# Kernel optimization log

Hardware: AMD Instinct MI355X
Metric: run time of the kernel (lower is better)

Reference implementation:

```python
import jax, jax.numpy as jnp
import numpy as np

N = 262144          # batch size
C = 100             # num_classes
R0, R1 = 0.95, 1.0  # recall_range
LAM = 0.5           # lambda_pauc
LS = 0.1            # label_smoothing
MAX_PAUC = R1 - R0


def setup_inputs() -> dict:
    key = jax.random.key(0)
    k1, k2 = jax.random.split(key)
    predictions = jax.random.normal(k1, (N, C), dtype=jnp.float32)
    targets = jax.random.randint(k2, (N,), 0, C)
    weight = jnp.ones((C,), dtype=jnp.float32)
    return {"predictions": predictions, "targets": targets, "weight": weight}


def _roc_curves(scores, labels):
    """Vectorized per-class ROC. scores, labels: [C, N].
    Replaces the O(N^2) per-threshold loop with sort + cumsum (tie-correct:
    tp at threshold s_j counts ALL samples with score >= s_j)."""
    order = jnp.argsort(-scores, axis=1)                      # descending
    ss = jnp.take_along_axis(scores, order, axis=1)           # [C, N]
    sl = jnp.take_along_axis(labels, order, axis=1)           # [C, N]
    cpos = jnp.cumsum(sl, axis=1)                             # cumulative positives
    # last index within each tie-group of equal scores
    neg = -ss  # ascending
    idx = jax.vmap(lambda a: jnp.searchsorted(a, a, side='right'))(neg) - 1
    tp = jnp.take_along_axis(cpos, idx, axis=1)
    cnt = (idx + 1).astype(scores.dtype)
    fp = cnt - tp
    P = cpos[:, -1:]                       # total positives per class
    Nn = scores.shape[1] - P               # total negatives per class
    tpr = jnp.where(P > 0, tp / jnp.maximum(P, 1.0), 0.0)
    fpr = jnp.where(Nn > 0, fp / jnp.maximum(Nn, 1.0), 0.0)
    return fpr, tpr


def reference(predictions, targets, weight):
    probs = jax.nn.softmax(predictions, axis=1)               # [N, C]
    onehot = jnp.eye(C, dtype=predictions.dtype)[targets]     # [N, C]
    onehot_s = (1.0 - LS) * onehot + LS / C

    # per-class binary labels (smoothed true-class value > 0.5)
    labels = (onehot_s > 0.5).astype(predictions.dtype).T     # [C, N]
    scores = probs.T                                          # [C, N]

    fpr, tpr = _roc_curves(scores, labels)
    mask = (tpr >= R0) & (tpr <= R1)
    y = jnp.maximum(tpr - R0, 0.0)
    # tpr is monotone non-decreasing, so the recall mask is contiguous and
    # trapz over the masked subset == sum over adjacent pairs both in mask.
    pm = (mask[:, :-1] & mask[:, 1:]).astype(predictions.dtype)
    pauc = jnp.sum(0.5 * (y[:, :-1] + y[:, 1:]) * (fpr[:, 1:] - fpr[:, :-1]) * pm, axis=1)  # [C]

    avg_p_auc = jnp.sum(pauc * weight) / (jnp.sum(weight) * MAX_PAUC)
    # torch computes TP/FP via .item(): the pAUC path carries no gradient
    avg_p_auc = jax.lax.stop_gradient(jnp.clip(avg_p_auc, 0.0, 1.0))

    log_probs = jax.nn.log_softmax(predictions, axis=1)
    ce_loss = -jnp.mean(jnp.sum(onehot_s * log_probs * weight, axis=1))
    pauc_loss = 1.0 - avg_p_auc ** 2
    return (1.0 - LAM) * ce_loss + LAM * pauc_loss
```

## Files before the change

### kernel.cpp

```cpp
#include <hip/hip_runtime.h>
#include <math.h>

#define WAVE 64
constexpr int   CC      = 100;
constexpr int   MAXM    = 160;
constexpr int   BUCKET  = 4096;
constexpr int   USTRIDE = 161;
constexpr int   LCAP    = 4096;
constexpr float LSMOOTH = 0.1f;
constexpr int   TILE    = 64;

__global__ __launch_bounds__(256) void k1_tile(
    const float* __restrict__ pred, const int* __restrict__ targets,
    const float* __restrict__ weight, float* __restrict__ L_out,
    float* __restrict__ pos_out, float* __restrict__ ce_partial, int N)
{
    __shared__ float tile[TILE * CC];
    __shared__ int   ttgt[TILE];
    __shared__ float tL[TILE], tpos[TILE];
    __shared__ float cered[4];
    const int tid = threadIdx.x;
    const int r0  = blockIdx.x * TILE;

    const float4* src = (const float4*)(pred + (size_t)r0 * CC);
    #pragma unroll
    for (int t = tid; t < TILE * (CC / 4); t += 256)
        *((float4*)&tile[t * 4]) = src[t];
    if (tid < TILE) ttgt[tid] = targets[r0 + tid];
    __syncthreads();

    const int x = tid & 15;
    const int G = tid >> 4;
    float w[7];
    #pragma unroll
    for (int j = 0; j < 7; ++j) {
        int c = x + 16 * j;
        w[j] = (c < CC) ? weight[c] : 0.0f;
    }
    float Wl = 0.0f;
    #pragma unroll
    for (int j = 0; j < 7; ++j) Wl += w[j];
    #pragma unroll
    for (int off = 1; off < 16; off <<= 1) Wl += __shfl_xor(Wl, off, 16);

    float ce_acc = 0.0f;
    #pragma unroll
    for (int rr = 0; rr < 4; ++rr) {
        const int r = G * 4 + rr;
        const float* rp = tile + r * CC;
        float v[7];
        #pragma unroll
        for (int j = 0; j < 7; ++j) {
            int c = x + 16 * j;
            v[j] = (c < CC) ? rp[c] : -INFINITY;
        }
        float vmax = v[0];
        #pragma unroll
        for (int j = 1; j < 7; ++j) vmax = fmaxf(vmax, v[j]);
        #pragma unroll
        for (int off = 1; off < 16; off <<= 1) vmax = fmaxf(vmax, __shfl_xor(vmax, off, 16));
        float z = 0.0f, ws = 0.0f;
        #pragma unroll
        for (int j = 0; j < 7; ++j) {
            int c = x + 16 * j;
            if (c < CC) { z += __expf(v[j] - vmax); ws += w[j] * v[j]; }
        }
        #pragma unroll
        for (int off = 1; off < 16; off <<= 1) {
            z  += __shfl_xor(z,  off, 16);
            ws += __shfl_xor(ws, off, 16);
        }
        float L = vmax + __logf(z);
        if (x == 0) {
            int t = ttgt[r];
            float pt = rp[t];
            tL[r] = L; tpos[r] = pt - L;
            ce_acc += -((1.0f - LSMOOTH) * weight[t] * (pt - L)
                        + (LSMOOTH / CC) * (ws - Wl * L));
        }
    }
    #pragma unroll
    for (int off = 32; off; off >>= 1) ce_acc += __shfl_xor(ce_acc, off, WAVE);
    if ((tid & 63) == 0) cered[tid >> 6] = ce_acc;
    __syncthreads();
    if (tid < TILE) {
        L_out[r0 + tid]   = tL[tid];
        pos_out[r0 + tid] = tpos[tid];
    }
    if (tid == 0)
        ce_partial[blockIdx.x] = cered[0] + cered[1] + cered[2] + cered[3];
}

__global__ __launch_bounds__(256) void k1b_scatter(
    const int* __restrict__ targets, const float* __restrict__ pos,
    int* __restrict__ cls_cnt, float* __restrict__ bucket, int N)
{
    __shared__ int hist[CC];
    __shared__ int base[CC];
    __shared__ int loc[CC];
    const int tid = threadIdx.x;
    const int rowsPerBlock = N / gridDim.x;
    const int r0 = blockIdx.x * rowsPerBlock;
    const int r1 = r0 + rowsPerBlock;
    for (int c = tid; c < CC; c += blockDim.x) { hist[c] = 0; loc[c] = 0; }
    __syncthreads();
    for (int r = r0 + tid; r < r1; r += blockDim.x)
        atomicAdd(&hist[targets[r]], 1);
    __syncthreads();
    for (int c = tid; c < CC; c += blockDim.x)
        base[c] = (hist[c] > 0) ? atomicAdd(&cls_cnt[c], hist[c]) : 0;
    __syncthreads();
    for (int r = r0 + tid; r < r1; r += blockDim.x) {
        int c = targets[r];
        int idx = base[c] + atomicAdd(&loc[c], 1);
        if (idx < BUCKET) bucket[(size_t)c * BUCKET + idx] = pos[r];
    }
}

__global__ __launch_bounds__(256) void k2_select(
    const float* __restrict__ bucket, const int* __restrict__ cls_cnt,
    float* __restrict__ u, int* __restrict__ m_arr, int* __restrict__ P_arr,
    float* __restrict__ wm_arr)
{
    __shared__ unsigned int keys[BUCKET];
    __shared__ unsigned int hist[256];
    __shared__ unsigned int scan[256];
    __shared__ unsigned int sel[256];
    __shared__ unsigned int s_prefix;
    __shared__ int s_rank;
    __shared__ int cnt_lt;
    const int c   = blockIdx.x;
    const int tid = threadIdx.x;
    const int P = min(cls_cnt[c], BUCKET);
    double Kd = 0.95 * (double)P;
    int kf = (int)floor(Kd);
    int m = P - kf;
    if (m > MAXM) m = MAXM;
    if (m < 0) m = 0;
    if (tid == 0) {
        m_arr[c] = m; P_arr[c] = P;
        wm_arr[c] = (float)((double)(kf + 1) - Kd);
        s_prefix = 0; s_rank = m - 1; cnt_lt = 0;
    }
    for (int i = tid; i < P; i += 256) {
        unsigned int b = __float_as_uint(bucket[(size_t)c * BUCKET + i]);
        keys[i] = (b & 0x80000000u) ? ~b : (b | 0x80000000u);
    }
    __syncthreads();
    if (m == 0) return;

    for (int shift = 24; shift >= 0; shift -= 8) {
        hist[tid] = 0;
        __syncthreads();
        unsigned int pref = s_prefix;
        for (int i = tid; i < P; i += 256) {
            unsigned int k = keys[i];
            bool match = (shift == 24) || ((k >> (shift + 8)) == pref);
            if (match) atomicAdd(&hist[(k >> shift) & 255u], 1u);
        }
        __syncthreads();
        scan[tid] = hist[tid];
        __syncthreads();
        for (int off = 1; off < 256; off <<= 1) {
            unsigned int add = (tid >= off) ? scan[tid - off] : 0u;
            __syncthreads();
            scan[tid] += add;
            __syncthreads();
        }
        int r = s_rank;
        unsigned int inc = scan[tid];
        unsigned int exc = inc - hist[tid];
        __syncthreads();
        if ((unsigned int)r >= exc && (unsigned int)r < inc) {
            s_rank   = r - (int)exc;
            s_prefix = (pref << 8) | (unsigned int)tid;
        }
        __syncthreads();
    }
    const unsigned int kth = s_prefix;

    for (int i = tid; i < P; i += 256) {
        unsigned int k = keys[i];
        if (k < kth) {
            int pslot = atomicAdd(&cnt_lt, 1);
            sel[pslot] = k;
        }
    }
    __syncthreads();
    const int nlt = cnt_lt;
    for (int j = nlt + tid; j < 256; j += 256) sel[j] = (j < m) ? kth : 0xFFFFFFFFu;
    __syncthreads();
    for (int kk = 2; kk <= 256; kk <<= 1) {
        for (int j = kk >> 1; j > 0; j >>= 1) {
            int i = tid, ixj = tid ^ j;
            if (ixj > i) {
                unsigned int a = sel[i], b = sel[ixj];
                bool up = ((i & kk) == 0);
                if ((a > b) == up) { sel[i] = b; sel[ixj] = a; }
            }
            __syncthreads();
        }
    }
    if (tid < m) {
        unsigned int k = sel[tid];
        unsigned int b = (k & 0x80000000u) ? (k & 0x7fffffffu) : ~k;
        u[c * MAXM + tid] = __uint_as_float(b);
    }
}

__device__ __forceinline__ int ubound(const float* uc, int m, float key, int maxidx) {
    int l = 0;
    #pragma unroll
    for (int s = 128; s; s >>= 1) {
        int p = l + s - 1;
        float val = uc[p < maxidx ? p : maxidx];
        l += ((p < m) && (val <= key)) ? s : 0;
    }
    return l;
}

__global__ __launch_bounds__(256) void k3a_stream(
    const float4* __restrict__ pred4, const float* __restrict__ L,
    const float* __restrict__ u, const int* __restrict__ m_arr,
    uint2* __restrict__ list, int* __restrict__ list_cnt, int list_cap,
    int* __restrict__ g_cnt, int* __restrict__ g_sum, int total4)
{
    __shared__ float umax_s[CC];
    __shared__ uint2 buf[LCAP];
    __shared__ int lcnt;
    __shared__ int gbase;
    const int tid = threadIdx.x;
    if (tid < CC) {
        int m = m_arr[tid];
        umax_s[tid] = (m > 0) ? u[tid * MAXM + m - 1] : -INFINITY;
    }
    if (tid == 0) lcnt = 0;
    __syncthreads();

    const int stride = gridDim.x * blockDim.x;
    int i = blockIdx.x * blockDim.x + tid;
    int j = i % 25;
    int n = i / 25;
    const int dj = stride % 25, dn = stride / 25;
    while (i < total4) {
        float4 v = pred4[i];
        float Ln = L[n];
        float4 um = *((const float4*)&umax_s[j * 4]);
        float s0 = v.x - Ln, s1 = v.y - Ln, s2 = v.z - Ln, s3 = v.w - Ln;
        #pragma unroll
        for (int q = 0; q < 4; ++q) {
            float sc = (q == 0) ? s0 : (q == 1) ? s1 : (q == 2) ? s2 : s3;
            float mx = (q == 0) ? um.x : (q == 1) ? um.y : (q == 2) ? um.z : um.w;
            if (sc < mx) {
                int c = j * 4 + q;
                int idx = atomicAdd(&lcnt, 1);
                if (idx < LCAP) {
                    buf[idx] = make_uint2((unsigned int)c, __float_as_uint(sc));
                } else {
                    int m = m_arr[c];
                    int l = ubound(u + c * MAXM, m, sc, MAXM - 1);
                    atomicAdd(&g_cnt[c], 1);
                    atomicAdd(&g_sum[c], m - 1 - l);
                }
            }
        }
        i += stride; j += dj; n += dn;
        if (j >= 25) { j -= 25; n += 1; }
    }
    __syncthreads();
    int cnt = min(lcnt, LCAP);
    if (tid == 0) gbase = atomicAdd(list_cnt, cnt);
    __syncthreads();
    const int base0 = gbase;
    for (int k = tid; k < cnt; k += 256) {
        int gi = base0 + k;
        if (gi < list_cap) {
            list[gi] = buf[k];
        } else {
            uint2 e = buf[k];
            int c = (int)e.x; float sc = __uint_as_float(e.y);
            int m = m_arr[c];
            int l = ubound(u + c * MAXM, m, sc, MAXM - 1);
            atomicAdd(&g_cnt[c], 1);
            atomicAdd(&g_sum[c], m - 1 - l);
        }
    }
}

__global__ __launch_bounds__(256) void k3b_rank(
    const uint2* __restrict__ list, const int* __restrict__ list_cnt, int list_cap,
    const float* __restrict__ u, const int* __restrict__ m_arr,
    int* __restrict__ g_cnt, int* __restrict__ g_sum)
{
    __shared__ float us[CC * USTRIDE];
    __shared__ int sm[CC];
    __shared__ int lcnt[CC], lsum[CC];
    const int tid = threadIdx.x;
    for (int c = tid; c < CC; c += 256) { sm[c] = m_arr[c]; lcnt[c] = 0; lsum[c] = 0; }
    for (int t = tid; t < CC * MAXM; t += 256) {
        int c = t / MAXM, k = t - c * MAXM;
        us[c * USTRIDE + k] = u[t];
    }
    __syncthreads();
    const int n = min(*list_cnt, list_cap);
    const int stride = gridDim.x * blockDim.x;
    for (int idx = blockIdx.x * blockDim.x + tid; idx < n; idx += stride) {
        uint2 e = list[idx];
        int c = (int)e.x;
        float key = __uint_as_float(e.y);
        int m = sm[c];
        int l = ubound(us + c * USTRIDE, m, key, USTRIDE - 1);
        atomicAdd(&lcnt[c], 1);
        atomicAdd(&lsum[c], m - 1 - l);
    }
    __syncthreads();
    for (int c = tid; c < CC; c += 256) {
        if (lcnt[c]) { atomicAdd(&g_cnt[c], lcnt[c]); atomicAdd(&g_sum[c], lsum[c]); }
    }
}

__global__ __launch_bounds__(256) void k4_final(
    const float* __restrict__ ce_partial, int nPartial,
    const float* __restrict__ weight, const int* __restrict__ P_arr,
    const int* __restrict__ m_arr, const float* __restrict__ wm_arr,
    const int* __restrict__ g_cnt, const int* __restrict__ g_sum,
    float* __restrict__ out, int N)
{
    __shared__ double r1[256], r2[256], r3[256];
    double ce = 0.0;
    for (int i = threadIdx.x; i < nPartial; i += blockDim.x) ce += (double)ce_partial[i];
    double p = 0.0, wsum = 0.0;
    for (int c = threadIdx.x; c < CC; c += blockDim.x) {
        int P = P_arr[c], m = m_arr[c];
        double wgt = (double)weight[c];
        long long Nn = (long long)N - P;
        if (P > 0 && Nn > 0 && m > 0) {
            double wm = (double)wm_arr[c];
            double S   = (double)g_sum[c] + wm * (double)g_cnt[c];
            double sub = 0.5 * (double)(m - 1) * (double)(m - 2) + wm * (double)(m - 1);
            double pc  = (S - sub) / ((double)Nn * (double)P);
            if (pc < 0.0) pc = 0.0;
            p += pc * wgt;
        }
        wsum += wgt;
    }
    r1[threadIdx.x] = ce; r2[threadIdx.x] = p; r3[threadIdx.x] = wsum;
    __syncthreads();
    for (int off = blockDim.x >> 1; off; off >>= 1) {
        if ((int)threadIdx.x < off) {
            r1[threadIdx.x] += r1[threadIdx.x + off];
            r2[threadIdx.x] += r2[threadIdx.x + off];
            r3[threadIdx.x] += r3[threadIdx.x + off];
        }
        __syncthreads();
    }
    if (threadIdx.x == 0) {
        double ce_loss = r1[0] / (double)N;
        double avg = r2[0] / (r3[0] * 0.05);
        avg = fmin(fmax(avg, 0.0), 1.0);
        out[0] = (float)(0.5 * ce_loss + 0.5 * (1.0 - avg * avg));
    }
}

extern "C" void kernel_launch(void* const* d_in, const int* in_sizes, int n_in,
                              void* d_out, int out_size, void* d_ws, size_t ws_size,
                              hipStream_t stream) {
    (void)n_in; (void)out_size;
    const float* pred    = (const float*)d_in[0];
    const int*   targets = (const int*)d_in[1];
    const float* weight  = (const float*)d_in[2];
    float* out = (float*)d_out;
    const int N = in_sizes[1];

    const int K1_BLOCKS = N / TILE;
    char* base = (char*)d_ws;
    size_t off = 0;
    auto take = [&](size_t bytes) { char* q = base + off; off += (bytes + 15) & ~(size_t)15; return q; };
    float* L_ws       = (float*)take((size_t)N * 4);
    float* pos_ws     = (float*)take((size_t)N * 4);
    float* ce_partial = (float*)take((size_t)K1_BLOCKS * 4);
    float* u          = (float*)take((size_t)CC * MAXM * 4);
    int*   m_arr      = (int*)take(CC * 4);
    int*   P_arr      = (int*)take(CC * 4);
    float* wm_arr     = (float*)take(CC * 4);
    int*   zero_blk   = (int*)take(304 * 4);
    int*   cls_cnt  = zero_blk;
    int*   g_cnt    = zero_blk + CC;
    int*   g_sum    = zero_blk + 2 * CC;
    int*   list_cnt = zero_blk + 3 * CC;
    float* bucket     = (float*)take((size_t)CC * BUCKET * 4);
    uint2* list       = (uint2*)(base + off);
    long long rem     = (long long)ws_size - (long long)off;
    int list_cap      = (rem > 0) ? (int)(rem / 8) : 0;

    hipMemsetAsync(zero_blk, 0, 304 * 4, stream);

    k1_tile<<<K1_BLOCKS, 256, 0, stream>>>(pred, targets, weight, L_ws, pos_ws,
                                           ce_partial, N);
    k1b_scatter<<<256, 256, 0, stream>>>(targets, pos_ws, cls_cnt, bucket, N);
    k2_select<<<CC, 256, 0, stream>>>(bucket, cls_cnt, u, m_arr, P_arr, wm_arr);
    const int total4 = (int)((size_t)N * CC / 4);
    k3a_stream<<<1024, 256, 0, stream>>>((const float4*)pred, L_ws, u, m_arr,
                                         list, list_cnt, list_cap, g_cnt, g_sum, total4);
    k3b_rank<<<512, 256, 0, stream>>>(list, list_cnt, list_cap, u, m_arr, g_cnt, g_sum);
    k4_final<<<1, 256, 0, stream>>>(ce_partial, K1_BLOCKS, weight, P_arr, m_arr, wm_arr,
                                    g_cnt, g_sum, out, N);
}
```

Measured before the change: 263.5 us.

## Fuse stream, rank and final kernels into one pass with last-block reduction

Merges the candidate-streaming kernel, the list-based ranking kernel and the final reduction into a single kernel. Each block preloads the per-class threshold tables into shared memory and ranks candidates inline with local atomics, dropping the global candidate list and its round trip. The last block to finish, found through an atomic counter, computes the final loss. The stream loop now issues four float4 loads per iteration to raise memory-level parallelism, and the radix-select prefix scan in k2 becomes a single-wave shuffle scan. The trade-offs are a larger shared-memory footprint per block, which lowers occupancy, and possible branch divergence from the inline binary search.

New measurement: 354.2 us. 1.34x slower.

```diff
diff --git a/kernel.cpp b/kernel.cpp
--- a/kernel.cpp
+++ b/kernel.cpp
@@ -6,9 +6,9 @@
 constexpr int   MAXM    = 160;
 constexpr int   BUCKET  = 4096;
 constexpr int   USTRIDE = 161;
-constexpr int   LCAP    = 4096;
 constexpr float LSMOOTH = 0.1f;
 constexpr int   TILE    = 64;
+constexpr int   K3GRID  = 512;
 
 __global__ __launch_bounds__(256) void k1_tile(
     const float* __restrict__ pred, const int* __restrict__ targets,
@@ -159,14 +159,23 @@
             if (match) atomicAdd(&hist[(k >> shift) & 255u], 1u);
         }
         __syncthreads();
-        scan[tid] = hist[tid];
-        __syncthreads();
-        for (int off = 1; off < 256; off <<= 1) {
-            unsigned int add = (tid >= off) ? scan[tid - off] : 0u;
-            __syncthreads();
-            scan[tid] += add;
-            __syncthreads();
-        }
+        if (tid < 64) {
+            unsigned h0 = hist[tid*4], h1 = hist[tid*4+1],
+                     h2 = hist[tid*4+2], h3 = hist[tid*4+3];
+            unsigned s0 = h0, s1 = s0 + h1, s2 = s1 + h2, s3 = s2 + h3;
+            unsigned sc = s3;
+            #pragma unroll
+            for (int off = 1; off < 64; off <<= 1) {
+                unsigned t2 = __shfl_up(sc, (unsigned)off, 64);
+                if (tid >= off) sc += t2;
+            }
+            unsigned excl = sc - s3;
+            scan[tid*4]   = excl + s0;
+            scan[tid*4+1] = excl + s1;
+            scan[tid*4+2] = excl + s2;
+            scan[tid*4+3] = excl + s3;
+        }
+        __syncthreads();
         int r = s_rank;
         unsigned int inc = scan[tid];
         unsigned int exc = inc - hist[tid];
@@ -219,124 +228,101 @@
     return l;
 }
 
-__global__ __launch_bounds__(256) void k3a_stream(
+__global__ __launch_bounds__(256) void k3_rank_final(
     const float4* __restrict__ pred4, const float* __restrict__ L,
     const float* __restrict__ u, const int* __restrict__ m_arr,
-    uint2* __restrict__ list, int* __restrict__ list_cnt, int list_cap,
-    int* __restrict__ g_cnt, int* __restrict__ g_sum, int total4)
-{
-    __shared__ float umax_s[CC];
-    __shared__ uint2 buf[LCAP];
-    __shared__ int lcnt;
-    __shared__ int gbase;
-    const int tid = threadIdx.x;
-    if (tid < CC) {
-        int m = m_arr[tid];
-        umax_s[tid] = (m > 0) ? u[tid * MAXM + m - 1] : -INFINITY;
-    }
-    if (tid == 0) lcnt = 0;
-    __syncthreads();
-
-    const int stride = gridDim.x * blockDim.x;
-    int i = blockIdx.x * blockDim.x + tid;
-    int j = i % 25;
-    int n = i / 25;
-    const int dj = stride % 25, dn = stride / 25;
-    while (i < total4) {
-        float4 v = pred4[i];
-        float Ln = L[n];
-        float4 um = *((const float4*)&umax_s[j * 4]);
-        float s0 = v.x - Ln, s1 = v.y - Ln, s2 = v.z - Ln, s3 = v.w - Ln;
-        #pragma unroll
-        for (int q = 0; q < 4; ++q) {
-            float sc = (q == 0) ? s0 : (q == 1) ? s1 : (q == 2) ? s2 : s3;
-            float mx = (q == 0) ? um.x : (q == 1) ? um.y : (q == 2) ? um.z : um.w;
-            if (sc < mx) {
-                int c = j * 4 + q;
-                int idx = atomicAdd(&lcnt, 1);
-                if (idx < LCAP) {
-                    buf[idx] = make_uint2((unsigned int)c, __float_as_uint(sc));
-                } else {
-                    int m = m_arr[c];
-                    int l = ubound(u + c * MAXM, m, sc, MAXM - 1);
-                    atomicAdd(&g_cnt[c], 1);
-                    atomicAdd(&g_sum[c], m - 1 - l);
-                }
-            }
-        }
-        i += stride; j += dj; n += dn;
-        if (j >= 25) { j -= 25; n += 1; }
-    }
-    __syncthreads();
-    int cnt = min(lcnt, LCAP);
-    if (tid == 0) gbase = atomicAdd(list_cnt, cnt);
-    __syncthreads();
-    const int base0 = gbase;
-    for (int k = tid; k < cnt; k += 256) {
-        int gi = base0 + k;
-        if (gi < list_cap) {
-            list[gi] = buf[k];
-        } else {
-            uint2 e = buf[k];
-            int c = (int)e.x; float sc = __uint_as_float(e.y);
-            int m = m_arr[c];
-            int l = ubound(u + c * MAXM, m, sc, MAXM - 1);
-            atomicAdd(&g_cnt[c], 1);
-            atomicAdd(&g_sum[c], m - 1 - l);
-        }
-    }
-}
-
-__global__ __launch_bounds__(256) void k3b_rank(
-    const uint2* __restrict__ list, const int* __restrict__ list_cnt, int list_cap,
-    const float* __restrict__ u, const int* __restrict__ m_arr,
-    int* __restrict__ g_cnt, int* __restrict__ g_sum)
+    const int* __restrict__ P_arr, const float* __restrict__ wm_arr,
+    const float* __restrict__ weight, const float* __restrict__ ce_partial,
+    int nPartial, int* __restrict__ g_cnt, int* __restrict__ g_sum,
+    int* __restrict__ done, float* __restrict__ out, int N)
 {
     __shared__ float us[CC * USTRIDE];
-    __shared__ int sm[CC];
-    __shared__ int lcnt[CC], lsum[CC];
+    __shared__ float umax_s[CC];
+    __shared__ int   sm[CC], lcnt[CC], lsum[CC];
+    __shared__ int   lastflag;
+    __shared__ double r1[256], r2[256], r3[256];
     const int tid = threadIdx.x;
-    for (int c = tid; c < CC; c += 256) { sm[c] = m_arr[c]; lcnt[c] = 0; lsum[c] = 0; }
+
+    for (int c = tid; c < CC; c += 256) {
+        int m = m_arr[c];
+        sm[c] = m; lcnt[c] = 0; lsum[c] = 0;
+        umax_s[c] = (m > 0) ? u[c * MAXM + m - 1] : -INFINITY;
+    }
     for (int t = tid; t < CC * MAXM; t += 256) {
         int c = t / MAXM, k = t - c * MAXM;
         us[c * USTRIDE + k] = u[t];
     }
     __syncthreads();
-    const int n = min(*list_cnt, list_cap);
-    const int stride = gridDim.x * blockDim.x;
-    for (int idx = blockIdx.x * blockDim.x + tid; idx < n; idx += stride) {
-        uint2 e = list[idx];
-        int c = (int)e.x;
-        float key = __uint_as_float(e.y);
-        int m = sm[c];
-        int l = ubound(us + c * USTRIDE, m, key, USTRIDE - 1);
-        atomicAdd(&lcnt[c], 1);
-        atomicAdd(&lsum[c], m - 1 - l);
-    }
-    __syncthreads();
+
+    const int total4 = N * (CC / 4);
+    const int stride = K3GRID * 256;
+
+    auto proc = [&](float4 v, float Ln, int j) {
+        float4 um = *((const float4*)&umax_s[j * 4]);
+        float s0 = v.x - Ln, s1 = v.y - Ln, s2 = v.z - Ln, s3 = v.w - Ln;
+        #pragma unroll
+        for (int q = 0; q < 4; ++q) {
+            float scv = (q == 0) ? s0 : (q == 1) ? s1 : (q == 2) ? s2 : s3;
+            float mx  = (q == 0) ? um.x : (q == 1) ? um.y : (q == 2) ? um.z : um.w;
+            if (scv < mx) {
+                int c = j * 4 + q;
+                int m = sm[c];
+                int l = ubound(us + c * USTRIDE, m, scv, USTRIDE - 1);
+                atomicAdd(&lcnt[c], 1);
+                atomicAdd(&lsum[c], m - 1 - l);
+            }
+        }
+    };
+
+    int i = blockIdx.x * 256 + tid;
+    while (i < total4) {
+        const int ia = i + stride, ib = i + 2 * stride, ic = i + 3 * stride;
+        const bool ha = ia < total4, hb = ib < total4, hc = ic < total4;
+        float4 v0 = pred4[i];
+        float4 va = ha ? pred4[ia] : make_float4(0.f, 0.f, 0.f, 0.f);
+        float4 vb = hb ? pred4[ib] : make_float4(0.f, 0.f, 0.f, 0.f);
+        float4 vc = hc ? pred4[ic] : make_float4(0.f, 0.f, 0.f, 0.f);
+        int n0 = i / 25,  j0 = i - n0 * 25;
+        float L0 = L[n0];
+        int na = 0, ja = 0, nb = 0, jb = 0, nc = 0, jc = 0;
+        float La = 0.f, Lb = 0.f, Lc = 0.f;
+        if (ha) { na = ia / 25; ja = ia - na * 25; La = L[na]; }
+        if (hb) { nb = ib / 25; jb = ib - nb * 25; Lb = L[nb]; }
+        if (hc) { nc = ic / 25; jc = ic - nc * 25; Lc = L[nc]; }
+        proc(v0, L0, j0);
+        if (ha) proc(va, La, ja);
+        if (hb) proc(vb, Lb, jb);
+        if (hc) proc(vc, Lc, jc);
+        i += 4 * stride;
+    }
+    __syncthreads();
+
+    for (int c = tid; c < CC; c += 256)
+        if (lcnt[c]) {
+            atomicAdd(&g_cnt[c], lcnt[c]);
+            atomicAdd(&g_sum[c], lsum[c]);
+        }
+    __threadfence();
+    __syncthreads();
+    if (tid == 0) {
+        int r = atomicAdd(done, 1);
+        lastflag = (r == (int)gridDim.x - 1) ? 1 : 0;
+    }
+    __syncthreads();
+    if (!lastflag) return;
+
+    double ce = 0.0;
+    for (int t = tid; t < nPartial; t += 256) ce += (double)ce_partial[t];
+    double p = 0.0, wsum = 0.0;
     for (int c = tid; c < CC; c += 256) {
-        if (lcnt[c]) { atomicAdd(&g_cnt[c], lcnt[c]); atomicAdd(&g_sum[c], lsum[c]); }
-    }
-}
-
-__global__ __launch_bounds__(256) void k4_final(
-    const float* __restrict__ ce_partial, int nPartial,
-    const float* __restrict__ weight, const int* __restrict__ P_arr,
-    const int* __restrict__ m_arr, const float* __restrict__ wm_arr,
-    const int* __restrict__ g_cnt, const int* __restrict__ g_sum,
-    float* __restrict__ out, int N)
-{
-    __shared__ double r1[256], r2[256], r3[256];
-    double ce = 0.0;
-    for (int i = threadIdx.x; i < nPartial; i += blockDim.x) ce += (double)ce_partial[i];
-    double p = 0.0, wsum = 0.0;
-    for (int c = threadIdx.x; c < CC; c += blockDim.x) {
         int P = P_arr[c], m = m_arr[c];
         double wgt = (double)weight[c];
         long long Nn = (long long)N - P;
         if (P > 0 && Nn > 0 && m > 0) {
+            int gc = __hip_atomic_load(&g_cnt[c], __ATOMIC_RELAXED, __HIP_MEMORY_SCOPE_AGENT);
+            int gs = __hip_atomic_load(&g_sum[c], __ATOMIC_RELAXED, __HIP_MEMORY_SCOPE_AGENT);
             double wm = (double)wm_arr[c];
-            double S   = (double)g_sum[c] + wm * (double)g_cnt[c];
+            double S   = (double)gs + wm * (double)gc;
             double sub = 0.5 * (double)(m - 1) * (double)(m - 2) + wm * (double)(m - 1);
             double pc  = (S - sub) / ((double)Nn * (double)P);
             if (pc < 0.0) pc = 0.0;
@@ -344,17 +330,17 @@
         }
         wsum += wgt;
     }
-    r1[threadIdx.x] = ce; r2[threadIdx.x] = p; r3[threadIdx.x] = wsum;
-    __syncthreads();
-    for (int off = blockDim.x >> 1; off; off >>= 1) {
-        if ((int)threadIdx.x < off) {
-            r1[threadIdx.x] += r1[threadIdx.x + off];
-            r2[threadIdx.x] += r2[threadIdx.x + off];
-            r3[threadIdx.x] += r3[threadIdx.x + off];
-        }
-        __syncthreads();
-    }
-    if (threadIdx.x == 0) {
+    r1[tid] = ce; r2[tid] = p; r3[tid] = wsum;
+    __syncthreads();
+    for (int off = 128; off; off >>= 1) {
+        if (tid < off) {
+            r1[tid] += r1[tid + off];
+            r2[tid] += r2[tid + off];
+            r3[tid] += r3[tid + off];
+        }
+        __syncthreads();
+    }
+    if (tid == 0) {
         double ce_loss = r1[0] / (double)N;
         double avg = r2[0] / (r3[0] * 0.05);
         avg = fmin(fmax(avg, 0.0), 1.0);
@@ -365,7 +351,7 @@
 extern "C" void kernel_launch(void* const* d_in, const int* in_sizes, int n_in,
                               void* d_out, int out_size, void* d_ws, size_t ws_size,
                               hipStream_t stream) {
-    (void)n_in; (void)out_size;
+    (void)n_in; (void)out_size; (void)ws_size;
     const float* pred    = (const float*)d_in[0];
     const int*   targets = (const int*)d_in[1];
     const float* weight  = (const float*)d_in[2];
@@ -387,11 +373,8 @@
     int*   cls_cnt  = zero_blk;
     int*   g_cnt    = zero_blk + CC;
     int*   g_sum    = zero_blk + 2 * CC;
-    int*   list_cnt = zero_blk + 3 * CC;
+    int*   done     = zero_blk + 3 * CC;
     float* bucket     = (float*)take((size_t)CC * BUCKET * 4);
-    uint2* list       = (uint2*)(base + off);
-    long long rem     = (long long)ws_size - (long long)off;
-    int list_cap      = (rem > 0) ? (int)(rem / 8) : 0;
 
     hipMemsetAsync(zero_blk, 0, 304 * 4, stream);
 
@@ -399,10 +382,7 @@
                                            ce_partial, N);
     k1b_scatter<<<256, 256, 0, stream>>>(targets, pos_ws, cls_cnt, bucket, N);
     k2_select<<<CC, 256, 0, stream>>>(bucket, cls_cnt, u, m_arr, P_arr, wm_arr);
-    const int total4 = (int)((size_t)N * CC / 4);
-    k3a_stream<<<1024, 256, 0, stream>>>((const float4*)pred, L_ws, u, m_arr,
-                                         list, list_cnt, list_cap, g_cnt, g_sum, total4);
-    k3b_rank<<<512, 256, 0, stream>>>(list, list_cnt, list_cap, u, m_arr, g_cnt, g_sum);
-    k4_final<<<1, 256, 0, stream>>>(ce_partial, K1_BLOCKS, weight, P_arr, m_arr, wm_arr,
-                                    g_cnt, g_sum, out, N);
-}
+    k3_rank_final<<<K3GRID, 256, 0, stream>>>((const float4*)pred, L_ws, u, m_arr,
+                                              P_arr, wm_arr, weight, ce_partial,
+                                              K1_BLOCKS, g_cnt, g_sum, done, out, N);
+}
```
